# Optimization experiments

Hardware: AMD Instinct MI355X
Metric: run time of the kernel (lower is better)

Reference implementation:

```python
import jax, jax.numpy as jnp
import numpy as np

N_S = 50000   # support points
N_Q = 50000   # query points
H = 32        # neighbors per query
K = 15        # kernel points
C_IN = 64
C_OUT = 64
G = 8         # group norm groups
RADIUS = 1.0
SIGMA = 0.6
EPS = 1e-5
NEG_SLOPE = 0.1


def setup_inputs() -> dict:
    key = jax.random.key(0)
    ks = jax.random.split(key, 8)
    s_feats = jax.random.normal(ks[0], (N_S, C_IN), jnp.float32)
    q_points = jax.random.uniform(ks[1], (N_Q, 3), jnp.float32)
    s_points = jax.random.uniform(ks[2], (N_S, 3), jnp.float32)
    # index N_S is the shadow (padding) neighbor
    neighbor_indices = jax.random.randint(ks[3], (N_Q, H), 0, N_S + 1)
    # kernel point dispositions: fixed points inside a ball of RADIUS
    d = jax.random.normal(ks[4], (K, 3), jnp.float32)
    d = d / jnp.linalg.norm(d, axis=1, keepdims=True)
    r = jax.random.uniform(ks[5], (K, 1), jnp.float32) ** (1.0 / 3.0)
    kernel_points = d * r * RADIUS                      # (K,3)
    weights = jax.random.normal(ks[6], (K, C_IN, C_OUT), jnp.float32) * (1.0 / np.sqrt(K * C_IN))
    bias = jax.random.normal(ks[7], (C_OUT,), jnp.float32) * 0.01
    gamma = jnp.ones((C_OUT,), jnp.float32)
    beta = jnp.zeros((C_OUT,), jnp.float32)
    return dict(s_feats=s_feats, q_points=q_points, s_points=s_points,
                neighbor_indices=neighbor_indices, kernel_points=kernel_points,
                weights=weights, bias=bias, gamma=gamma, beta=beta)


def kpconv(s_feats, q_points, s_points, neighbor_indices, kernel_points, weights, bias):
    # pad support set with shadow point (1e10) and zero features
    pad_pts = jnp.concatenate([s_points, jnp.full((1, 3), 1e10, s_points.dtype)], axis=0)
    pad_feats = jnp.concatenate([s_feats, jnp.zeros((1, s_feats.shape[1]), s_feats.dtype)], axis=0)
    nbr_pts = pad_pts[neighbor_indices] - q_points[:, None, :]              # (M,H,3)
    diff = nbr_pts[:, :, None, :] - kernel_points[None, None, :, :]         # (M,H,K,3)
    sq_d = jnp.sum(diff * diff, axis=-1)                                    # (M,H,K)
    # linear correlation influence, clamped at 0
    w = jnp.maximum(1.0 - jnp.sqrt(sq_d) / SIGMA, 0.0)                      # (M,H,K)
    nbr_feats = pad_feats[neighbor_indices]                                 # (M,H,Cin)
    weighted = jnp.einsum('mhk,mhc->mkc', w, nbr_feats)                     # (M,K,Cin)
    out = jnp.einsum('mkc,kcd->md', weighted, weights)                      # (M,Cout)
    # normalize by number of valid neighbors (feature-sum > 0 test, as in KPConv)
    nbr_num = jnp.sum(jnp.sum(nbr_feats, axis=-1) > 0, axis=-1)             # (M,)
    nbr_num = jnp.maximum(nbr_num, 1).astype(out.dtype)
    return out / nbr_num[:, None] + bias


def group_norm(x, gamma, beta):
    # matches GroupNorm wrapper: (M,C) -> (1,C,M) -> nn.GroupNorm -> (M,C)
    M, C = x.shape
    xg = x.T.reshape(G, C // G, M)                                          # (G,Cg,M)
    mean = xg.mean(axis=(1, 2), keepdims=True)
    var = xg.var(axis=(1, 2), keepdims=True)
    xn = ((xg - mean) / jnp.sqrt(var + EPS)).reshape(C, M).T                # (M,C)
    return xn * gamma + beta


def reference(s_feats, q_points, s_points, neighbor_indices, kernel_points, weights, bias, gamma, beta):
    x = kpconv(s_feats, q_points, s_points, neighbor_indices, kernel_points, weights, bias)
    x = group_norm(x, gamma, beta)
    x = jnp.where(x >= 0, x, NEG_SLOPE * x)                                 # LeakyReLU(0.1)
    return x[:, None, :]                                                    # unsqueeze(1): (M,1,Cout)
```

## Files before the change

kernel.cpp:

```cpp
#include <hip/hip_runtime.h>
#include <hip/hip_bf16.h>
#include <math.h>

#define NSUP 50000
#define NQ   50000
#define NH   32
#define NK   15
#define NG   8
#define INV_SIGMA (1.0f/0.6f)
#define GN_EPS 1e-5f
#define NEG  0.1f

#define QB   16
#define NBLK (NQ/QB)

#define OFF_ROWSUM 0
#define OFF_FB     50048
#define OFF_WB     (OFF_FB + 1600000)
#define OFF_PS     (OFF_WB + 30720)
#define OFF_PQ     (OFF_PS + NBLK*8)
#define OFF_STAT   (OFF_PQ + NBLK*8)

typedef __attribute__((ext_vector_type(8))) short bf16x8;
typedef __attribute__((ext_vector_type(4))) float f32x4;
typedef __attribute__((ext_vector_type(4))) unsigned int u32x4;

__device__ __forceinline__ short f2bf(float x) {
    __hip_bfloat16 h = __float2bfloat16(x);
    return *reinterpret_cast<short*>(&h);
}

__global__ __launch_bounds__(256) void k_prep(const float* __restrict__ sf,
                                              float* __restrict__ rowsum,
                                              unsigned short* __restrict__ fb,
                                              const float* __restrict__ wts,
                                              unsigned short* __restrict__ wb) {
    if (blockIdx.x < 12500) {
        int row  = (blockIdx.x * 256 + threadIdx.x) >> 6;
        int lane = threadIdx.x & 63;
        if (row >= NSUP) return;
        float v = sf[(size_t)row * 64 + lane];
        fb[(size_t)row * 64 + lane] = (unsigned short)f2bf(v);
        float s = v;
        #pragma unroll
        for (int o = 32; o; o >>= 1) s += __shfl_down(s, o);
        if (lane == 0) rowsum[row] = s;
    } else {
        int idx = (blockIdx.x - 12500) * 256 + threadIdx.x;
        if (idx >= 30 * 4 * 64 * 8) return;
        int j  = idx & 7;
        int l  = (idx >> 3) & 63;
        int n  = (idx >> 9) & 3;
        int ks = idx >> 11;
        int r  = ks * 32 + ((l >> 4) << 3) + j;
        int d  = n * 16 + (l & 15);
        wb[idx] = (unsigned short)f2bf(wts[(size_t)r * 64 + d]);
    }
}

__global__ __launch_bounds__(256, 5) void k_conv(
    const unsigned short* __restrict__ fb, const float* __restrict__ qpts,
    const float* __restrict__ spts,  const int*   __restrict__ nidx,
    const float* __restrict__ kpts,  const unsigned short* __restrict__ wb,
    const float* __restrict__ bias,  const float* __restrict__ rowsum,
    float* __restrict__ conv_out, float* __restrict__ part_s, float* __restrict__ part_q)
{
    __shared__ __align__(16) short wl16[16 * 968];
    __shared__ __align__(16) float kp4[16][4];
    __shared__ float rcl[16];

    const int tid  = threadIdx.x;
    const int wv   = tid >> 6;
    const int lane = tid & 63;
    const int g    = lane >> 4;
    const int c16  = lane & 15;

    if (tid < 16) {
        if (tid < NK) {
            kp4[tid][0] = kpts[tid*3+0];
            kp4[tid][1] = kpts[tid*3+1];
            kp4[tid][2] = kpts[tid*3+2];
        } else {
            kp4[tid][0] = 1e8f; kp4[tid][1] = 1e8f; kp4[tid][2] = 1e8f;
        }
        kp4[tid][3] = 0.f;
    }
    __syncthreads();

    const float kx = kp4[c16][0], ky = kp4[c16][1], kz = kp4[c16][2];

    const int qbase = blockIdx.x * QB;
    char* FP = (char*)wl16 + wv * 6144;

    f32x4 pacc[4][4];
    #pragma unroll
    for (int a = 0; a < 4; a++)
        #pragma unroll
        for (int b = 0; b < 4; b++) pacc[a][b] = (f32x4){0.f,0.f,0.f,0.f};

    const int h    = lane & 31;
    const int half = lane >> 5;

    float dxr[2], dyr[2], dzr[2];
    #pragma unroll
    for (int pp = 0; pp < 2; pp++) {
        const int qq = pp*2 + half;
        const int m  = qbase + wv*4 + qq;
        const float qx = qpts[m*3+0], qy = qpts[m*3+1], qz = qpts[m*3+2];
        const int  id  = nidx[(size_t)m * NH + h];
        const bool val = (id < NSUP);
        const int  ii  = val ? id : 0;
        const float dx = spts[ii*3+0]-qx, dy = spts[ii*3+1]-qy, dz = spts[ii*3+2]-qz;
        const float rs = rowsum[ii];
        unsigned long long bal = __ballot(val && rs > 0.f);
        int cA = __popcll(bal & 0xffffffffull); if (cA < 1) cA = 1;
        int cB = __popcll(bal >> 32);           if (cB < 1) cB = 1;
        if (lane == 0)  rcl[wv*4 + pp*2]     = 1.0f / (float)cA;
        if (lane == 32) rcl[wv*4 + pp*2 + 1] = 1.0f / (float)cB;
        dxr[pp] = val ? dx : 1e10f; dyr[pp] = dy; dzr[pp] = dz;
    }

    const int gr = lane >> 3;
    const int gs = lane & 7;
    int   idp[4];
    u32x4 vp[4];
    {
        const int m0 = qbase + wv*4;
        #pragma unroll
        for (int i = 0; i < 4; i++) idp[i] = nidx[(size_t)m0*NH + i*8 + gr];
        #pragma unroll
        for (int i = 0; i < 4; i++) {
            const int id2 = (idp[i] < NSUP) ? idp[i] : 0;
            vp[i] = *(const u32x4*)((const char*)fb + (size_t)id2*128 + gs*16);
        }
    }

    #pragma unroll
    for (int q = 0; q < 4; q++) {
        const int pp = q >> 1, e = q & 1;

        #pragma unroll
        for (int i = 0; i < 4; i++)
            *(u32x4*)(FP + (i*8 + gr)*144 + ((gs ^ i) << 4)) = vp[i];

        if (q < 3) {
            const int mn = qbase + wv*4 + q + 1;
            #pragma unroll
            for (int i = 0; i < 4; i++) idp[i] = nidx[(size_t)mn*NH + i*8 + gr];
        }

        union { unsigned short u[8]; bf16x8 v; } ua;
        #pragma unroll
        for (int j = 0; j < 8; j++) {
            const int sl = e*32 + g*8 + j;
            const float px = __shfl(dxr[pp], sl);
            const float py = __shfl(dyr[pp], sl);
            const float pz = __shfl(dzr[pp], sl);
            const float ex = px - kx, ey = py - ky, ez = pz - kz;
            const float sq = fmaf(ex, ex, fmaf(ey, ey, ez * ez));
            const float w  = fmaxf(1.0f - sqrtf(sq) * INV_SIGMA, 0.f);
            ua.u[j] = (unsigned short)f2bf(w);
        }

        if (q < 3) {
            #pragma unroll
            for (int i = 0; i < 4; i++) {
                const int id2 = (idp[i] < NSUP) ? idp[i] : 0;
                vp[i] = *(const u32x4*)((const char*)fb + (size_t)id2*128 + gs*16);
            }
        }

        #pragma unroll
        for (int ct = 0; ct < 4; ct++) {
            const char* vb = FP + (g*8)*144
                           + (((((ct << 1) | (c16 >> 3)) ^ g) & 7) << 4)
                           + ((c16 & 7) << 1);
            union { unsigned short u[8]; bf16x8 v; } ub;
            #pragma unroll
            for (int j = 0; j < 8; j++)
                ub.u[j] = *(const unsigned short*)(vb + j*144);
            pacc[q][ct] = __builtin_amdgcn_mfma_f32_16x16x32_bf16(ua.v, ub.v, pacc[q][ct], 0, 0, 0);
        }
    }

    __syncthreads();

    #pragma unroll
    for (int qq = 0; qq < 4; qq++) {
        #pragma unroll
        for (int ct = 0; ct < 4; ct++) {
            #pragma unroll
            for (int i = 0; i < 4; i++) {
                const int kk = g*4 + i;
                if (kk < NK) {
                    const int ch = kk*8 + ct*2 + (c16 >> 3);
                    const int sc = ch ^ ((ch >> 5) & 3);
                    wl16[(wv*4 + qq)*968 + sc*8 + (c16 & 7)] = f2bf(pacc[qq][ct][i]);
                }
            }
        }
    }
    __syncthreads();

    f32x4 facc = (f32x4){0.f,0.f,0.f,0.f};
    const int z = lane >> 4;
    const short* arow = wl16 + c16*968;
    const unsigned short* bp = wb + ((size_t)(wv * 64 + lane)) * 8;
    #pragma unroll 6
    for (int ks = 0; ks < 30; ks++) {
        const int L  = ks*4 + z;
        const int sL = L ^ ((L >> 5) & 3);
        bf16x8 a = *(const bf16x8*)(arow + sL*8);
        bf16x8 b = *(const bf16x8*)(bp + (size_t)ks*2048);
        facc = __builtin_amdgcn_mfma_f32_16x16x32_bf16(a, b, facc, 0, 0, 0);
    }

    const int   d  = wv*16 + c16;
    const float bs = bias[d];
    float gl = 0.f, gq = 0.f;
    #pragma unroll
    for (int i = 0; i < 4; i++) {
        const int row = z*4 + i;
        const float y = facc[i] * rcl[row] + bs;
        conv_out[(size_t)(qbase + row)*64 + d] = y;
        gl += y;
        gq = fmaf(y, y, gq);
    }
    #pragma unroll
    for (int msk = 1; msk <= 4; msk <<= 1) { gl += __shfl_xor(gl, msk); gq += __shfl_xor(gq, msk); }
    gl += __shfl_xor(gl, 16); gq += __shfl_xor(gq, 16);
    gl += __shfl_xor(gl, 32); gq += __shfl_xor(gq, 32);
    if ((lane & 55) == 0) {
        const int grp = wv*2 + (lane >> 3);
        part_s[(size_t)blockIdx.x * 8 + grp] = gl;
        part_q[(size_t)blockIdx.x * 8 + grp] = gq;
    }
}

__global__ __launch_bounds__(1024) void k_reduce(const float* __restrict__ part_s,
                                                 const float* __restrict__ part_q,
                                                 float* __restrict__ stat) {
    __shared__ double ds[128][8], dq[128][8];
    const int t = threadIdx.x;
    const int g = t & 7, chunk = t >> 3;
    const int per = (NBLK + 127) / 128;
    double s = 0.0, q = 0.0;
    int lo = chunk * per, hi = lo + per; if (hi > NBLK) hi = NBLK;
    for (int i = lo; i < hi; i++) {
        s += (double)part_s[(size_t)i * 8 + g];
        q += (double)part_q[(size_t)i * 8 + g];
    }
    ds[chunk][g] = s; dq[chunk][g] = q;
    __syncthreads();
    if (t < 8) {
        double S = 0.0, Q = 0.0;
        for (int cix = 0; cix < 128; cix++) { S += ds[cix][t]; Q += dq[cix][t]; }
        const double cnt = (double)(64 / NG) * (double)NQ;
        double mean = S / cnt;
        double var  = Q / cnt - mean * mean;
        stat[t]     = (float)mean;
        stat[8 + t] = (float)(1.0 / sqrt(var + (double)GN_EPS));
    }
}

__global__ __launch_bounds__(256) void k_apply(float* __restrict__ out,
                                               const float* __restrict__ stat,
                                               const float* __restrict__ gamma,
                                               const float* __restrict__ beta) {
    const int n4 = NQ * 64 / 4;
    for (int idx = blockIdx.x * 256 + threadIdx.x; idx < n4; idx += gridDim.x * 256) {
        float4 v = ((const float4*)out)[idx];
        const int c4 = idx & 15;
        const int g  = c4 >> 1;
        const float mean = stat[g], istd = stat[8 + g];
        const float4 ga = ((const float4*)gamma)[c4];
        const float4 be = ((const float4*)beta)[c4];
        float4 r;
        r.x = (v.x - mean) * istd * ga.x + be.x; r.x = r.x >= 0.f ? r.x : NEG * r.x;
        r.y = (v.y - mean) * istd * ga.y + be.y; r.y = r.y >= 0.f ? r.y : NEG * r.y;
        r.z = (v.z - mean) * istd * ga.z + be.z; r.z = r.z >= 0.f ? r.z : NEG * r.z;
        r.w = (v.w - mean) * istd * ga.w + be.w; r.w = r.w >= 0.f ? r.w : NEG * r.w;
        ((float4*)out)[idx] = r;
    }
}

extern "C" void kernel_launch(void* const* d_in, const int* in_sizes, int n_in,
                              void* d_out, int out_size, void* d_ws, size_t ws_size,
                              hipStream_t stream) {
    const float* sfeats = (const float*)d_in[0];
    const float* qpts   = (const float*)d_in[1];
    const float* spts   = (const float*)d_in[2];
    const int*   nidx   = (const int*)  d_in[3];
    const float* kpts   = (const float*)d_in[4];
    const float* wts    = (const float*)d_in[5];
    const float* bias   = (const float*)d_in[6];
    const float* gamma  = (const float*)d_in[7];
    const float* beta   = (const float*)d_in[8];

    float* ws = (float*)d_ws;
    float*          rowsum = ws + OFF_ROWSUM;
    unsigned short* fb     = (unsigned short*)(ws + OFF_FB);
    unsigned short* wb     = (unsigned short*)(ws + OFF_WB);
    float*          ps     = ws + OFF_PS;
    float*          pq     = ws + OFF_PQ;
    float*          stat   = ws + OFF_STAT;
    float*          out    = (float*)d_out;

    k_prep <<<dim3(12740), dim3(256), 0, stream>>>(sfeats, rowsum, fb, wts, wb);
    k_conv <<<dim3(NBLK),  dim3(256), 0, stream>>>(fb, qpts, spts, nidx, kpts,
                                                   wb, bias, rowsum, out, ps, pq);
    k_reduce<<<dim3(1),    dim3(1024), 0, stream>>>(ps, pq, stat);
    k_apply <<<dim3(1024), dim3(256), 0, stream>>>(out, stat, gamma, beta);
}
```

Measured before the change: 81.47 us.

## Double-buffer neighbor feature gathers with direct global-to-LDS async loads

Neighbor feature rows are now loaded straight from global memory into LDS with global_load_lds instead of passing through registers. Two LDS buffers per wave let the gather for the next query overlap the MFMA work on the current one. The index prefetch runs two queries ahead, and the LDS row stride drops from 144 to 128 bytes, with XOR swizzling applied on the source address. Shared memory grows to 32 KB and the occupancy hint drops from 5 to 4 blocks, so fewer blocks may be resident and the hand-written waitcnt logic must be exactly right.

Result: slower. 85.51 us (+5.0%).

```diff
diff --git a/kernel.cpp b/kernel.cpp
--- a/kernel.cpp
+++ b/kernel.cpp
@@ -23,11 +23,16 @@
 
 typedef __attribute__((ext_vector_type(8))) short bf16x8;
 typedef __attribute__((ext_vector_type(4))) float f32x4;
-typedef __attribute__((ext_vector_type(4))) unsigned int u32x4;
 
 __device__ __forceinline__ short f2bf(float x) {
     __hip_bfloat16 h = __float2bfloat16(x);
     return *reinterpret_cast<short*>(&h);
+}
+
+__device__ __forceinline__ void g2l16(const void* g, void* l) {
+    __builtin_amdgcn_global_load_lds(
+        (const __attribute__((address_space(1))) unsigned int*)g,
+        (__attribute__((address_space(3))) unsigned int*)l, 16, 0, 0);
 }
 
 __global__ __launch_bounds__(256) void k_prep(const float* __restrict__ sf,
@@ -58,14 +63,14 @@
     }
 }
 
-__global__ __launch_bounds__(256, 5) void k_conv(
+__global__ __launch_bounds__(256, 4) void k_conv(
     const unsigned short* __restrict__ fb, const float* __restrict__ qpts,
     const float* __restrict__ spts,  const int*   __restrict__ nidx,
     const float* __restrict__ kpts,  const unsigned short* __restrict__ wb,
     const float* __restrict__ bias,  const float* __restrict__ rowsum,
     float* __restrict__ conv_out, float* __restrict__ part_s, float* __restrict__ part_q)
 {
-    __shared__ __align__(16) short wl16[16 * 968];
+    __shared__ __align__(16) char U[32768];
     __shared__ __align__(16) float kp4[16][4];
     __shared__ float rcl[16];
 
@@ -90,7 +95,8 @@
     const float kx = kp4[c16][0], ky = kp4[c16][1], kz = kp4[c16][2];
 
     const int qbase = blockIdx.x * QB;
-    char* FP = (char*)wl16 + wv * 6144;
+    char* FPa = U + wv * 8192;
+    char* FPb = FPa + 4096;
 
     f32x4 pacc[4][4];
     #pragma unroll
@@ -122,31 +128,47 @@
 
     const int gr = lane >> 3;
     const int gs = lane & 7;
-    int   idp[4];
-    u32x4 vp[4];
+    int ia[4];
+
     {
         const int m0 = qbase + wv*4;
         #pragma unroll
-        for (int i = 0; i < 4; i++) idp[i] = nidx[(size_t)m0*NH + i*8 + gr];
+        for (int i = 0; i < 4; i++) ia[i] = nidx[(size_t)m0*NH + i*8 + gr];
         #pragma unroll
         for (int i = 0; i < 4; i++) {
-            const int id2 = (idp[i] < NSUP) ? idp[i] : 0;
-            vp[i] = *(const u32x4*)((const char*)fb + (size_t)id2*128 + gs*16);
-        }
+            const int id2 = (ia[i] < NSUP) ? ia[i] : 0;
+            g2l16((const char*)fb + (size_t)id2*128 + ((gs ^ i) << 4), FPa + i*1024);
+        }
+        const int m1 = qbase + wv*4 + 1;
+        #pragma unroll
+        for (int i = 0; i < 4; i++) ia[i] = nidx[(size_t)m1*NH + i*8 + gr];
     }
 
     #pragma unroll
     for (int q = 0; q < 4; q++) {
         const int pp = q >> 1, e = q & 1;
-
-        #pragma unroll
-        for (int i = 0; i < 4; i++)
-            *(u32x4*)(FP + (i*8 + gr)*144 + ((gs ^ i) << 4)) = vp[i];
+        char* cur = (q & 1) ? FPb : FPa;
+        char* nxt = (q & 1) ? FPa : FPb;
+
+        asm volatile("s_waitcnt lgkmcnt(0)" ::: "memory");
+        __builtin_amdgcn_sched_barrier(0);
 
         if (q < 3) {
-            const int mn = qbase + wv*4 + q + 1;
             #pragma unroll
-            for (int i = 0; i < 4; i++) idp[i] = nidx[(size_t)mn*NH + i*8 + gr];
+            for (int i = 0; i < 4; i++) {
+                const int id2 = (ia[i] < NSUP) ? ia[i] : 0;
+                g2l16((const char*)fb + (size_t)id2*128 + ((gs ^ i) << 4), nxt + i*1024);
+            }
+            asm volatile("s_waitcnt vmcnt(4)" ::: "memory");
+        } else {
+            asm volatile("s_waitcnt vmcnt(0)" ::: "memory");
+        }
+        __builtin_amdgcn_sched_barrier(0);
+
+        if (q < 2) {
+            const int mn = qbase + wv*4 + q + 2;
+            #pragma unroll
+            for (int i = 0; i < 4; i++) ia[i] = nidx[(size_t)mn*NH + i*8 + gr];
         }
 
         union { unsigned short u[8]; bf16x8 v; } ua;
@@ -162,29 +184,22 @@
             ua.u[j] = (unsigned short)f2bf(w);
         }
 
-        if (q < 3) {
-            #pragma unroll
-            for (int i = 0; i < 4; i++) {
-                const int id2 = (idp[i] < NSUP) ? idp[i] : 0;
-                vp[i] = *(const u32x4*)((const char*)fb + (size_t)id2*128 + gs*16);
-            }
-        }
-
         #pragma unroll
         for (int ct = 0; ct < 4; ct++) {
-            const char* vb = FP + (g*8)*144
+            const char* vb = cur + g*1024
                            + (((((ct << 1) | (c16 >> 3)) ^ g) & 7) << 4)
                            + ((c16 & 7) << 1);
             union { unsigned short u[8]; bf16x8 v; } ub;
             #pragma unroll
             for (int j = 0; j < 8; j++)
-                ub.u[j] = *(const unsigned short*)(vb + j*144);
+                ub.u[j] = *(const unsigned short*)(vb + j*128);
             pacc[q][ct] = __builtin_amdgcn_mfma_f32_16x16x32_bf16(ua.v, ub.v, pacc[q][ct], 0, 0, 0);
         }
     }
 
     __syncthreads();
 
+    short* wl16 = (short*)U;
     #pragma unroll
     for (int qq = 0; qq < 4; qq++) {
         #pragma unroll
```

## Double-buffer neighbor feature gathers, stage offsets in LDS, drop store swizzle

Applied to the files above, without the earlier changes.

Neighbor feature gathers become double-buffered (vA/vB) and the index loads are issued two queries ahead, so global gather latency overlaps more compute. Relative neighbor coordinates are written to a per-wave LDS scratch and read back instead of broadcast with cross-lane shuffles. The XOR swizzle on the intermediate bf16 tile store and load is removed in favour of direct linear indexing. This costs more registers for the second buffer and a larger per-wave LDS footprint, and the unswizzled layout may bring back bank conflicts.

Result: faster. 77.80 us (-4.5%).

```diff
diff --git a/kernel.cpp b/kernel.cpp
--- a/kernel.cpp
+++ b/kernel.cpp
@@ -90,7 +90,9 @@
     const float kx = kp4[c16][0], ky = kp4[c16][1], kz = kp4[c16][2];
 
     const int qbase = blockIdx.x * QB;
-    char* FP = (char*)wl16 + wv * 6144;
+    char*  WV  = (char*)wl16 + wv * 7424;
+    float* XYP = (float*)WV;
+    char*  FP  = WV + 2560;
 
     f32x4 pacc[4][4];
     #pragma unroll
@@ -101,7 +103,6 @@
     const int h    = lane & 31;
     const int half = lane >> 5;
 
-    float dxr[2], dyr[2], dzr[2];
     #pragma unroll
     for (int pp = 0; pp < 2; pp++) {
         const int qq = pp*2 + half;
@@ -117,57 +118,64 @@
         int cB = __popcll(bal >> 32);           if (cB < 1) cB = 1;
         if (lane == 0)  rcl[wv*4 + pp*2]     = 1.0f / (float)cA;
         if (lane == 32) rcl[wv*4 + pp*2 + 1] = 1.0f / (float)cB;
-        dxr[pp] = val ? dx : 1e10f; dyr[pp] = dy; dzr[pp] = dz;
+        const int si = (pp*64 + half*32 + h) * 5;
+        XYP[si]     = val ? dx : 1e10f;
+        XYP[si + 1] = dy;
+        XYP[si + 2] = dz;
     }
 
     const int gr = lane >> 3;
     const int gs = lane & 7;
-    int   idp[4];
-    u32x4 vp[4];
+    int   idA[4], idB[4];
+    u32x4 vA[4], vB[4];
     {
         const int m0 = qbase + wv*4;
         #pragma unroll
-        for (int i = 0; i < 4; i++) idp[i] = nidx[(size_t)m0*NH + i*8 + gr];
+        for (int i = 0; i < 4; i++) idA[i] = nidx[(size_t)m0*NH + i*8 + gr];
         #pragma unroll
         for (int i = 0; i < 4; i++) {
-            const int id2 = (idp[i] < NSUP) ? idp[i] : 0;
-            vp[i] = *(const u32x4*)((const char*)fb + (size_t)id2*128 + gs*16);
-        }
+            const int id2 = (idA[i] < NSUP) ? idA[i] : 0;
+            vA[i] = *(const u32x4*)((const char*)fb + (size_t)id2*128 + gs*16);
+        }
+        const int m1 = qbase + wv*4 + 1;
+        #pragma unroll
+        for (int i = 0; i < 4; i++) idB[i] = nidx[(size_t)m1*NH + i*8 + gr];
     }
 
     #pragma unroll
     for (int q = 0; q < 4; q++) {
         const int pp = q >> 1, e = q & 1;
+        u32x4* vc  = (q & 1) ? vB  : vA;
+        u32x4* vn  = (q & 1) ? vA  : vB;
+        int*   idn = (q & 1) ? idA : idB;
+        int*   idt = (q & 1) ? idB : idA;
 
         #pragma unroll
         for (int i = 0; i < 4; i++)
-            *(u32x4*)(FP + (i*8 + gr)*144 + ((gs ^ i) << 4)) = vp[i];
+            *(u32x4*)(FP + (i*8 + gr)*144 + ((gs ^ i) << 4)) = vc[i];
 
         if (q < 3) {
-            const int mn = qbase + wv*4 + q + 1;
             #pragma unroll
-            for (int i = 0; i < 4; i++) idp[i] = nidx[(size_t)mn*NH + i*8 + gr];
+            for (int i = 0; i < 4; i++) {
+                const int id2 = (idn[i] < NSUP) ? idn[i] : 0;
+                vn[i] = *(const u32x4*)((const char*)fb + (size_t)id2*128 + gs*16);
+            }
+        }
+        if (q < 2) {
+            const int mn = qbase + wv*4 + q + 2;
+            #pragma unroll
+            for (int i = 0; i < 4; i++) idt[i] = nidx[(size_t)mn*NH + i*8 + gr];
         }
 
         union { unsigned short u[8]; bf16x8 v; } ua;
         #pragma unroll
         for (int j = 0; j < 8; j++) {
-            const int sl = e*32 + g*8 + j;
-            const float px = __shfl(dxr[pp], sl);
-            const float py = __shfl(dyr[pp], sl);
-            const float pz = __shfl(dzr[pp], sl);
+            const int xi = (pp*64 + e*32 + g*8 + j) * 5;
+            const float px = XYP[xi], py = XYP[xi+1], pz = XYP[xi+2];
             const float ex = px - kx, ey = py - ky, ez = pz - kz;
             const float sq = fmaf(ex, ex, fmaf(ey, ey, ez * ez));
             const float w  = fmaxf(1.0f - sqrtf(sq) * INV_SIGMA, 0.f);
             ua.u[j] = (unsigned short)f2bf(w);
-        }
-
-        if (q < 3) {
-            #pragma unroll
-            for (int i = 0; i < 4; i++) {
-                const int id2 = (idp[i] < NSUP) ? idp[i] : 0;
-                vp[i] = *(const u32x4*)((const char*)fb + (size_t)id2*128 + gs*16);
-            }
         }
 
         #pragma unroll
@@ -192,11 +200,8 @@
             #pragma unroll
             for (int i = 0; i < 4; i++) {
                 const int kk = g*4 + i;
-                if (kk < NK) {
-                    const int ch = kk*8 + ct*2 + (c16 >> 3);
-                    const int sc = ch ^ ((ch >> 5) & 3);
-                    wl16[(wv*4 + qq)*968 + sc*8 + (c16 & 7)] = f2bf(pacc[qq][ct][i]);
-                }
+                if (kk < NK)
+                    wl16[(wv*4 + qq)*968 + kk*64 + ct*16 + c16] = f2bf(pacc[qq][ct][i]);
             }
         }
     }
@@ -204,13 +209,11 @@
 
     f32x4 facc = (f32x4){0.f,0.f,0.f,0.f};
     const int z = lane >> 4;
-    const short* arow = wl16 + c16*968;
+    const short* ap = wl16 + c16*968 + z*8;
     const unsigned short* bp = wb + ((size_t)(wv * 64 + lane)) * 8;
     #pragma unroll 6
     for (int ks = 0; ks < 30; ks++) {
-        const int L  = ks*4 + z;
-        const int sL = L ^ ((L >> 5) & 3);
-        bf16x8 a = *(const bf16x8*)(arow + sL*8);
+        bf16x8 a = *(const bf16x8*)(ap + ks*32);
         bf16x8 b = *(const bf16x8*)(bp + (size_t)ks*2048);
         facc = __builtin_amdgcn_mfma_f32_16x16x32_bf16(a, b, facc, 0, 0, 0);
     }
```
